# Performance work log

Measured on AMD Instinct MI355X. Metric: run time of the kernel, lower is better.

## Reference

```python
import jax, jax.numpy as jnp
import numpy as np

N_NODES = 50000


def gcn_conv(x, row, col, W, b):
    """PyG GCNConv: add self-loops, symmetric deg^-1/2 normalization,
    linear transform, scatter-add aggregation, bias.
    Self-loop contribution is added analytically (norm = dinv[i]^2)
    instead of appending edges."""
    n = x.shape[0]
    h = x @ W  # [N, out]
    # degree over edges-with-self-loops, counted at target (col)
    deg = jnp.zeros((n,), dtype=x.dtype).at[col].add(1.0) + 1.0
    dinv = jax.lax.rsqrt(deg)  # deg >= 1 thanks to self-loops
    norm = dinv[row] * dinv[col]  # [E]
    # neighbor aggregation: out[col] += norm * h[row]
    agg = jnp.zeros_like(h).at[col].add(norm[:, None] * h[row])
    # self-loop term: dinv[i]^2 * h[i]
    agg = agg + (dinv * dinv)[:, None] * h
    return agg + b


def setup_inputs() -> dict:
    key = jax.random.key(0)
    ks = jax.random.split(key, 8)
    d_in, d_hid, d_out = 128, 128, 128
    n_edges = 625000
    x = jax.random.normal(ks[0], (N_NODES, d_in), dtype=jnp.float32)
    edge_index = jax.random.randint(ks[1], (2, n_edges), 0, N_NODES, dtype=jnp.int64)
    # Glorot-style weights, zero bias (PyG GCNConv defaults)
    def glorot(k, fan_in, fan_out):
        s = jnp.sqrt(6.0 / (fan_in + fan_out)).astype(jnp.float32)
        return jax.random.uniform(k, (fan_in, fan_out), dtype=jnp.float32, minval=-s, maxval=s)
    return {
        "x": x,
        "edge_index": edge_index,
        "W1": glorot(ks[2], d_in, d_hid), "b1": jnp.zeros((d_hid,), jnp.float32),
        "W2": glorot(ks[3], d_hid, d_hid), "b2": jnp.zeros((d_hid,), jnp.float32),
        "W3": glorot(ks[4], d_hid, d_out), "b3": jnp.zeros((d_out,), jnp.float32),
    }


def reference(x, edge_index, W1, b1, W2, b2, W3, b3):
    row, col = edge_index[0], edge_index[1]
    h = jax.nn.relu(gcn_conv(x, row, col, W1, b1))
    h = jax.nn.relu(gcn_conv(h, row, col, W2, b2))
    out = gcn_conv(h, row, col, W3, b3)  # no ReLU on last layer
    return out
```

## Files before the change

### kernel.cpp

```cpp
#include <hip/hip_runtime.h>
#include <hip/hip_fp16.h>

#define NN 50000
#define NE 625000
#define D 128
#define SCAN_BLK 1024
#define NSB ((NN + SCAN_BLK - 1) / SCAN_BLK)

typedef _Float16 half8 __attribute__((ext_vector_type(8)));
typedef float f32x4 __attribute__((ext_vector_type(4)));

union H8U4 { _Float16 h[8]; uint4 u; };


__global__ void zero_kernel(int4* __restrict__ p) {
    int i = blockIdx.x * blockDim.x + threadIdx.x;
    if (i < NN / 4 + 1) p[i] = make_int4(0, 0, 0, 0);
}

__global__ void count_kernel(const int* __restrict__ col, int* __restrict__ counts) {
    int i = blockIdx.x * blockDim.x + threadIdx.x;
    if (i < NE) atomicAdd(&counts[col[i]], 1);
}

__global__ __launch_bounds__(256) void scan1_kernel(const int* __restrict__ counts,
                                                    int* __restrict__ excl,
                                                    int* __restrict__ blocksums) {
    const int b = blockIdx.x, t = threadIdx.x;
    const int base = b * SCAN_BLK + t * 4;
    int v0 = 0, v1 = 0, v2 = 0, v3 = 0;
    if (base + 3 < NN) {
        int4 c = *(const int4*)(counts + base);
        v0 = c.x; v1 = c.y; v2 = c.z; v3 = c.w;
    } else {
        if (base     < NN) v0 = counts[base];
        if (base + 1 < NN) v1 = counts[base + 1];
        if (base + 2 < NN) v2 = counts[base + 2];
        if (base + 3 < NN) v3 = counts[base + 3];
    }
    const int s = v0 + v1 + v2 + v3;
    const int lane = t & 63, wid = t >> 6;
    int inc = s;
    #pragma unroll
    for (int off = 1; off < 64; off <<= 1) {
        int n = __shfl_up(inc, off, 64);
        if (lane >= off) inc += n;
    }
    __shared__ int wsum[4];
    if (lane == 63) wsum[wid] = inc;
    __syncthreads();
    int wbase = 0;
    for (int w = 0; w < wid; w++) wbase += wsum[w];
    const int texcl = wbase + inc - s;
    if (base     < NN) excl[base]     = texcl;
    if (base + 1 < NN) excl[base + 1] = texcl + v0;
    if (base + 2 < NN) excl[base + 2] = texcl + v0 + v1;
    if (base + 3 < NN) excl[base + 3] = texcl + v0 + v1 + v2;
    if (t == 255) blocksums[b] = wbase + inc;
}

__global__ __launch_bounds__(64) void scan2_kernel(const int* __restrict__ blocksums,
                                                   int* __restrict__ blockoff) {
    const int t = threadIdx.x;
    int v = (t < NSB) ? blocksums[t] : 0;
    int inc = v;
    #pragma unroll
    for (int off = 1; off < 64; off <<= 1) {
        int n = __shfl_up(inc, off, 64);
        if (t >= off) inc += n;
    }
    if (t < NSB) blockoff[t] = inc - v;
}

__global__ void scan3_kernel(const int* __restrict__ counts, const int* __restrict__ excl,
                             const int* __restrict__ blockoff, int* __restrict__ offsets,
                             int* __restrict__ cursor, float* __restrict__ dinv) {
    const int i = blockIdx.x * blockDim.x + threadIdx.x;
    if (i < NN) {
        const int o = excl[i] + blockoff[i >> 10];
        offsets[i] = o;
        cursor[i] = o;
        dinv[i] = rsqrtf((float)counts[i] + 1.0f);
    }
    if (i == 0) offsets[NN] = NE;
}

__global__ void fill_kernel(const int* __restrict__ row, const int* __restrict__ col,
                            const float* __restrict__ dinv, int* __restrict__ cursor,
                            uint32_t* __restrict__ csr) {
    int i = blockIdx.x * blockDim.x + threadIdx.x;
    if (i < NE) {
        int r = row[i], c = col[i];
        int p = atomicAdd(&cursor[c], 1);
        __half hw = __float2half_rn(dinv[r] * dinv[c]);
        csr[p] = (uint32_t)r | ((uint32_t)*(const unsigned short*)&hw << 16);
    }
}


__global__ __launch_bounds__(256) void wpack3_kernel(const float* __restrict__ W1,
                                                     const float* __restrict__ W2,
                                                     const float* __restrict__ W3,
                                                     uint4* __restrict__ wp) {
    const int b = blockIdx.x;
    const float* W = (b < 8) ? W1 : (b < 16) ? W2 : W3;
    uint4* dst = wp + (size_t)(b >> 3) * 2048;
    int t = (b & 7) * 256 + threadIdx.x;
    int lane = t & 63, entry = t >> 6;
    int ks = entry >> 3, ctg = entry & 7;
    int j = ctg * 16 + (lane & 15);
    int kb = ks * 32 + (lane >> 4) * 8;
    H8U4 u;
    #pragma unroll
    for (int e = 0; e < 8; e++) u.h[e] = (_Float16)W[(kb + e) * 128 + j];
    dst[t] = u.u;
}


template <bool IN_F16>
__global__ __launch_bounds__(256) void gemm_mfma(const void* __restrict__ Ain,
                                                 const uint4* __restrict__ wpack,
                                                 uint32_t* __restrict__ Hh) {
    __shared__ alignas(16) _Float16 Cs[64][152];
    const int t = threadIdx.x;
    const int w = t >> 6, l = t & 63;
    const int row0 = blockIdx.x * 64;
    const int lr = l & 15;
    const int lg = l >> 4;

    int arow[4];
    #pragma unroll
    for (int rt = 0; rt < 4; rt++) {
        int gr = row0 + rt * 16 + lr;
        arow[rt] = (gr < NN) ? gr : NN - 1;
    }

    f32x4 acc[4][2];
    #pragma unroll
    for (int rt = 0; rt < 4; rt++)
        #pragma unroll
        for (int ct = 0; ct < 2; ct++)
            acc[rt][ct] = (f32x4){0.f, 0.f, 0.f, 0.f};

    #pragma unroll
    for (int ks = 0; ks < 4; ks++) {
        const int kbase = ks * 32 + lg * 8;
        half8 af[4];
        if (IN_F16) {
            const uint4* A = (const uint4*)Ain;
            #pragma unroll
            for (int rt = 0; rt < 4; rt++) {
                H8U4 u;
                u.u = A[arow[rt] * 16 + (kbase >> 3)];
                af[rt] = *(half8*)u.h;
            }
        } else {
            const float4* A = (const float4*)Ain;
            #pragma unroll
            for (int rt = 0; rt < 4; rt++) {
                float4 p0 = A[arow[rt] * 32 + (kbase >> 2)];
                float4 p1 = A[arow[rt] * 32 + (kbase >> 2) + 1];
                half8 h;
                h[0] = (_Float16)p0.x; h[1] = (_Float16)p0.y;
                h[2] = (_Float16)p0.z; h[3] = (_Float16)p0.w;
                h[4] = (_Float16)p1.x; h[5] = (_Float16)p1.y;
                h[6] = (_Float16)p1.z; h[7] = (_Float16)p1.w;
                af[rt] = h;
            }
        }
        half8 bf[2];
        #pragma unroll
        for (int ct = 0; ct < 2; ct++) {
            H8U4 u;
            u.u = wpack[(ks * 8 + (w * 2 + ct)) * 64 + l];
            bf[ct] = *(half8*)u.h;
        }
        #pragma unroll
        for (int rt = 0; rt < 4; rt++)
            #pragma unroll
            for (int ct = 0; ct < 2; ct++)
                acc[rt][ct] = __builtin_amdgcn_mfma_f32_16x16x32_f16(
                    af[rt], bf[ct], acc[rt][ct], 0, 0, 0);
    }

    #pragma unroll
    for (int rt = 0; rt < 4; rt++)
        #pragma unroll
        for (int ct = 0; ct < 2; ct++) {
            const int col = w * 32 + ct * 16 + lr;
            #pragma unroll
            for (int r = 0; r < 4; r++)
                Cs[rt * 16 + lg * 4 + r][col] = (_Float16)acc[rt][ct][r];
        }
    __syncthreads();

    #pragma unroll
    for (int i = t; i < 1024; i += 256) {
        const int row = i >> 4, c16 = i & 15;
        if (row0 + row < NN) {
            uint4 u = *(const uint4*)&Cs[row][c16 * 8];
            *(uint4*)(Hh + (size_t)(row0 + row) * 64 + c16 * 4) = u;
        }
    }
}


static __device__ __forceinline__ void proc4(uint32_t rec, bool valid, int lg,
                                             const uint4* __restrict__ hh4,
                                             float* __restrict__ acc) {
    const int s = (int)(rec & 0xffffu);
    unsigned short wb = (unsigned short)(rec >> 16);
    const float w = valid ? __half2float(*(const __half*)&wb) : 0.0f;
    uint4 v = hh4[(size_t)s * 16 + lg];
    float2 f0 = __half22float2(*(const __half2*)&v.x);
    float2 f1 = __half22float2(*(const __half2*)&v.y);
    float2 f2 = __half22float2(*(const __half2*)&v.z);
    float2 f3 = __half22float2(*(const __half2*)&v.w);
    acc[0] += w * f0.x; acc[1] += w * f0.y;
    acc[2] += w * f1.x; acc[3] += w * f1.y;
    acc[4] += w * f2.x; acc[5] += w * f2.y;
    acc[6] += w * f3.x; acc[7] += w * f3.y;
}

template <bool OUT_F16>
__global__ __launch_bounds__(256) void agg_kernel(const uint4* __restrict__ hh4,
                                                  const int* __restrict__ offsets,
                                                  const uint32_t* __restrict__ csr,
                                                  const float* __restrict__ dinv,
                                                  const float* __restrict__ bias,
                                                  void* __restrict__ out,
                                                  const int relu) {
    const int node = blockIdx.x * 4 + (threadIdx.x >> 6);
    if (node >= NN) return;
    const int l = threadIdx.x & 63;
    const int g = l >> 4;
    const int lg = l & 15;
    const float di = dinv[node];
    const float sw = di * di;
    const int e0 = offsets[node];
    const int e1 = offsets[node + 1];

    float a0[8], a1[8];
    #pragma unroll
    for (int i = 0; i < 8; i++) { a0[i] = 0.f; a1[i] = 0.f; }

    if (e0 < e1) {
        const int elast = e1 - 1;
        uint32_t r0 = csr[min(e0 + g, elast)];
        uint32_t r1 = csr[min(e0 + 4 + g, elast)];
        for (int eb = e0; eb < e1; eb += 8) {
            const int nb = eb + 8;
            uint32_t n0 = csr[min(nb + g, elast)];
            uint32_t n1 = csr[min(nb + 4 + g, elast)];
            proc4(r0, eb + g < e1, lg, hh4, a0);
            proc4(r1, eb + 4 + g < e1, lg, hh4, a1);
            r0 = n0; r1 = n1;
        }
    }

    float s[8];
    #pragma unroll
    for (int i = 0; i < 8; i++) s[i] = a0[i] + a1[i];
    #pragma unroll
    for (int i = 0; i < 8; i++) s[i] += __shfl_xor(s[i], 16, 64);
    #pragma unroll
    for (int i = 0; i < 8; i++) s[i] += __shfl_xor(s[i], 32, 64);

    uint4 sv = hh4[(size_t)node * 16 + lg];
    float2 f0 = __half22float2(*(const __half2*)&sv.x);
    float2 f1 = __half22float2(*(const __half2*)&sv.y);
    float2 f2 = __half22float2(*(const __half2*)&sv.z);
    float2 f3 = __half22float2(*(const __half2*)&sv.w);
    float4 b0 = ((const float4*)bias)[lg * 2];
    float4 b1 = ((const float4*)bias)[lg * 2 + 1];
    s[0] += sw * f0.x + b0.x; s[1] += sw * f0.y + b0.y;
    s[2] += sw * f1.x + b0.z; s[3] += sw * f1.y + b0.w;
    s[4] += sw * f2.x + b1.x; s[5] += sw * f2.y + b1.y;
    s[6] += sw * f3.x + b1.z; s[7] += sw * f3.y + b1.w;
    if (relu) {
        #pragma unroll
        for (int i = 0; i < 8; i++) s[i] = fmaxf(s[i], 0.f);
    }
    if (g == 0) {
        if (OUT_F16) {
            __half2 p0 = __float22half2_rn(make_float2(s[0], s[1]));
            __half2 p1 = __float22half2_rn(make_float2(s[2], s[3]));
            __half2 p2 = __float22half2_rn(make_float2(s[4], s[5]));
            __half2 p3 = __float22half2_rn(make_float2(s[6], s[7]));
            uint4 u;
            u.x = *(const uint32_t*)&p0;
            u.y = *(const uint32_t*)&p1;
            u.z = *(const uint32_t*)&p2;
            u.w = *(const uint32_t*)&p3;
            ((uint4*)out)[(size_t)node * 16 + lg] = u;
        } else {
            float4 o0 = make_float4(s[0], s[1], s[2], s[3]);
            float4 o1 = make_float4(s[4], s[5], s[6], s[7]);
            ((float4*)out)[(size_t)node * 32 + lg * 2] = o0;
            ((float4*)out)[(size_t)node * 32 + lg * 2 + 1] = o1;
        }
    }
}


extern "C" void kernel_launch(void* const* d_in, const int* in_sizes, int n_in,
                              void* d_out, int out_size, void* d_ws, size_t ws_size,
                              hipStream_t stream) {
    (void)in_sizes; (void)n_in; (void)out_size; (void)ws_size;
    const float* x  = (const float*)d_in[0];
    const int*   ei = (const int*)d_in[1];
    const float* W1 = (const float*)d_in[2];
    const float* b1 = (const float*)d_in[3];
    const float* W2 = (const float*)d_in[4];
    const float* b2 = (const float*)d_in[5];
    const float* W3 = (const float*)d_in[6];
    const float* b3 = (const float*)d_in[7];
    const int* row = ei;
    const int* col = ei + NE;
    float* outp = (float*)d_out;

    char* ws = (char*)d_ws;
    size_t off = 0;
    auto walloc = [&](size_t bytes) -> void* {
        void* p = ws + off;
        off = (off + bytes + 255) & ~(size_t)255;
        return p;
    };
    int*      counts   = (int*)walloc(NN * 4 + 16);
    int*      excl     = (int*)walloc(NN * 4);
    int*      blocksums= (int*)walloc(NSB * 4);
    int*      blockoff = (int*)walloc(NSB * 4);
    int*      offsets  = (int*)walloc((NN + 1) * 4);
    int*      cursor   = (int*)walloc(NN * 4);
    float*    dinv     = (float*)walloc(NN * 4);
    uint32_t* csr      = (uint32_t*)walloc((size_t)NE * 4);
    uint32_t* act16    = (uint32_t*)walloc((size_t)NN * D * 2);
    uint32_t* hh16     = (uint32_t*)walloc((size_t)NN * D * 2);
    uint4*    wp       = (uint4*)walloc(3 * 2048 * 16);

    zero_kernel<<<(NN / 4 + 1 + 255) / 256, 256, 0, stream>>>((int4*)counts);
    count_kernel<<<(NE + 255) / 256, 256, 0, stream>>>(col, counts);
    scan1_kernel<<<NSB, 256, 0, stream>>>(counts, excl, blocksums);
    scan2_kernel<<<1, 64, 0, stream>>>(blocksums, blockoff);
    scan3_kernel<<<(NN + 255) / 256, 256, 0, stream>>>(counts, excl, blockoff,
                                                       offsets, cursor, dinv);
    fill_kernel<<<(NE + 255) / 256, 256, 0, stream>>>(row, col, dinv, cursor, csr);
    wpack3_kernel<<<24, 256, 0, stream>>>(W1, W2, W3, wp);

    const int gblocks = (NN + 63) / 64;
    const int ablocks = (NN + 3) / 4;
    const uint4* hh4 = (const uint4*)hh16;
    gemm_mfma<false><<<gblocks, 256, 0, stream>>>(x, wp, hh16);
    agg_kernel<true><<<ablocks, 256, 0, stream>>>(hh4, offsets, csr, dinv, b1, act16, 1);
    gemm_mfma<true><<<gblocks, 256, 0, stream>>>(act16, wp + 2048, hh16);
    agg_kernel<true><<<ablocks, 256, 0, stream>>>(hh4, offsets, csr, dinv, b2, act16, 1);
    gemm_mfma<true><<<gblocks, 256, 0, stream>>>(act16, wp + 4096, hh16);
    agg_kernel<false><<<ablocks, 256, 0, stream>>>(hh4, offsets, csr, dinv, b3, outp, 0);
}
```

Measured before the change: 209.6 us.

## Split feature dimension into column slabs for cache-resident multi-pass aggregation

```diff
diff --git a/kernel.cpp b/kernel.cpp
--- a/kernel.cpp
+++ b/kernel.cpp
@@ -6,11 +6,13 @@
 #define D 128
 #define SCAN_BLK 1024
 #define NSB ((NN + SCAN_BLK - 1) / SCAN_BLK)
+#define NPASS 4
 
 typedef _Float16 half8 __attribute__((ext_vector_type(8)));
 typedef float f32x4 __attribute__((ext_vector_type(4)));
-
-union H8U4 { _Float16 h[8]; uint4 u; };
+typedef unsigned int u32x4 __attribute__((ext_vector_type(4)));
+
+union H8U4 { _Float16 h[8]; uint4 u; u32x4 v; };
 
 
 __global__ void zero_kernel(int4* __restrict__ p) {
@@ -120,7 +122,7 @@
 template <bool IN_F16>
 __global__ __launch_bounds__(256) void gemm_mfma(const void* __restrict__ Ain,
                                                  const uint4* __restrict__ wpack,
-                                                 uint32_t* __restrict__ Hh) {
+                                                 unsigned int* __restrict__ Hs) {
     __shared__ alignas(16) _Float16 Cs[64][152];
     const int t = threadIdx.x;
     const int w = t >> 6, l = t & 63;
@@ -144,17 +146,17 @@
 
     #pragma unroll
     for (int ks = 0; ks < 4; ks++) {
-        const int kbase = ks * 32 + lg * 8;
         half8 af[4];
         if (IN_F16) {
             const uint4* A = (const uint4*)Ain;
             #pragma unroll
             for (int rt = 0; rt < 4; rt++) {
                 H8U4 u;
-                u.u = A[arow[rt] * 16 + (kbase >> 3)];
+                u.u = A[(size_t)ks * NN * 4 + arow[rt] * 4 + lg];
                 af[rt] = *(half8*)u.h;
             }
         } else {
+            const int kbase = ks * 32 + lg * 8;
             const float4* A = (const float4*)Ain;
             #pragma unroll
             for (int rt = 0; rt < 4; rt++) {
@@ -198,20 +200,22 @@
     for (int i = t; i < 1024; i += 256) {
         const int row = i >> 4, c16 = i & 15;
         if (row0 + row < NN) {
-            uint4 u = *(const uint4*)&Cs[row][c16 * 8];
-            *(uint4*)(Hh + (size_t)(row0 + row) * 64 + c16 * 4) = u;
-        }
-    }
-}
-
-
-static __device__ __forceinline__ void proc4(uint32_t rec, bool valid, int lg,
-                                             const uint4* __restrict__ hh4,
-                                             float* __restrict__ acc) {
+            u32x4 u = *(const u32x4*)&Cs[row][c16 * 8];
+            u32x4* dst = (u32x4*)Hs + (size_t)(c16 >> 2) * NN * 4 +
+                         (size_t)(row0 + row) * 4 + (c16 & 3);
+            __builtin_nontemporal_store(u, dst);
+        }
+    }
+}
+
+
+static __device__ __forceinline__ void proc16(uint32_t rec, bool valid, int q,
+                                              const uint4* __restrict__ hsp,
+                                              float* __restrict__ acc) {
     const int s = (int)(rec & 0xffffu);
     unsigned short wb = (unsigned short)(rec >> 16);
     const float w = valid ? __half2float(*(const __half*)&wb) : 0.0f;
-    uint4 v = hh4[(size_t)s * 16 + lg];
+    uint4 v = hsp[(size_t)s * 4 + q];
     float2 f0 = __half22float2(*(const __half2*)&v.x);
     float2 f1 = __half22float2(*(const __half2*)&v.y);
     float2 f2 = __half22float2(*(const __half2*)&v.z);
@@ -223,18 +227,19 @@
 }
 
 template <bool OUT_F16>
-__global__ __launch_bounds__(256) void agg_kernel(const uint4* __restrict__ hh4,
-                                                  const int* __restrict__ offsets,
-                                                  const uint32_t* __restrict__ csr,
-                                                  const float* __restrict__ dinv,
-                                                  const float* __restrict__ bias,
-                                                  void* __restrict__ out,
-                                                  const int relu) {
+__global__ __launch_bounds__(256) void agg_pass(const uint4* __restrict__ hs,
+                                                const int* __restrict__ offsets,
+                                                const uint32_t* __restrict__ csr,
+                                                const float* __restrict__ dinv,
+                                                const float* __restrict__ bias,
+                                                void* __restrict__ out,
+                                                const int relu, const int pass) {
     const int node = blockIdx.x * 4 + (threadIdx.x >> 6);
     if (node >= NN) return;
     const int l = threadIdx.x & 63;
-    const int g = l >> 4;
-    const int lg = l & 15;
+    const int g = l >> 2;
+    const int q = l & 3;
+    const uint4* hsp = hs + (size_t)pass * NN * 4;
     const float di = dinv[node];
     const float sw = di * di;
     const int e0 = offsets[node];
@@ -246,14 +251,14 @@
 
     if (e0 < e1) {
         const int elast = e1 - 1;
-        uint32_t r0 = csr[min(e0 + g, elast)];
-        uint32_t r1 = csr[min(e0 + 4 + g, elast)];
-        for (int eb = e0; eb < e1; eb += 8) {
-            const int nb = eb + 8;
-            uint32_t n0 = csr[min(nb + g, elast)];
-            uint32_t n1 = csr[min(nb + 4 + g, elast)];
-            proc4(r0, eb + g < e1, lg, hh4, a0);
-            proc4(r1, eb + 4 + g < e1, lg, hh4, a1);
+        uint32_t r0 = __builtin_nontemporal_load(csr + min(e0 + g, elast));
+        uint32_t r1 = __builtin_nontemporal_load(csr + min(e0 + 16 + g, elast));
+        for (int eb = e0; eb < e1; eb += 32) {
+            const int nb = eb + 32;
+            uint32_t n0 = __builtin_nontemporal_load(csr + min(nb + g, elast));
+            uint32_t n1 = __builtin_nontemporal_load(csr + min(nb + 16 + g, elast));
+            proc16(r0, eb + g < e1, q, hsp, a0);
+            proc16(r1, eb + 16 + g < e1, q, hsp, a1);
             r0 = n0; r1 = n1;
         }
     }
@@ -262,17 +267,20 @@
     #pragma unroll
     for (int i = 0; i < 8; i++) s[i] = a0[i] + a1[i];
     #pragma unroll
-    for (int i = 0; i < 8; i++) s[i] += __shfl_xor(s[i], 16, 64);
-    #pragma unroll
-    for (int i = 0; i < 8; i++) s[i] += __shfl_xor(s[i], 32, 64);
-
-    uint4 sv = hh4[(size_t)node * 16 + lg];
+    for (int i = 0; i < 8; i++) {
+        s[i] += __shfl_xor(s[i], 4, 64);
+        s[i] += __shfl_xor(s[i], 8, 64);
+        s[i] += __shfl_xor(s[i], 16, 64);
+        s[i] += __shfl_xor(s[i], 32, 64);
+    }
+
+    uint4 sv = hsp[(size_t)node * 4 + q];
     float2 f0 = __half22float2(*(const __half2*)&sv.x);
     float2 f1 = __half22float2(*(const __half2*)&sv.y);
     float2 f2 = __half22float2(*(const __half2*)&sv.z);
     float2 f3 = __half22float2(*(const __half2*)&sv.w);
-    float4 b0 = ((const float4*)bias)[lg * 2];
-    float4 b1 = ((const float4*)bias)[lg * 2 + 1];
+    float4 b0 = ((const float4*)bias)[pass * 8 + q * 2];
+    float4 b1 = ((const float4*)bias)[pass * 8 + q * 2 + 1];
     s[0] += sw * f0.x + b0.x; s[1] += sw * f0.y + b0.y;
     s[2] += sw * f1.x + b0.z; s[3] += sw * f1.y + b0.w;
     s[4] += sw * f2.x + b1.x; s[5] += sw * f2.y + b1.y;
@@ -287,17 +295,19 @@
             __half2 p1 = __float22half2_rn(make_float2(s[2], s[3]));
             __half2 p2 = __float22half2_rn(make_float2(s[4], s[5]));
             __half2 p3 = __float22half2_rn(make_float2(s[6], s[7]));
-            uint4 u;
+            u32x4 u;
             u.x = *(const uint32_t*)&p0;
             u.y = *(const uint32_t*)&p1;
             u.z = *(const uint32_t*)&p2;
             u.w = *(const uint32_t*)&p3;
-            ((uint4*)out)[(size_t)node * 16 + lg] = u;
+            u32x4* dst = (u32x4*)out + (size_t)pass * NN * 4 + (size_t)node * 4 + q;
+            __builtin_nontemporal_store(u, dst);
         } else {
-            float4 o0 = make_float4(s[0], s[1], s[2], s[3]);
-            float4 o1 = make_float4(s[4], s[5], s[6], s[7]);
-            ((float4*)out)[(size_t)node * 32 + lg * 2] = o0;
-            ((float4*)out)[(size_t)node * 32 + lg * 2 + 1] = o1;
+            f32x4 o0 = {s[0], s[1], s[2], s[3]};
+            f32x4 o1 = {s[4], s[5], s[6], s[7]};
+            f32x4* dst = (f32x4*)out + (size_t)node * 32 + pass * 8 + q * 2;
+            __builtin_nontemporal_store(o0, dst);
+            __builtin_nontemporal_store(o1, dst + 1);
         }
     }
 }
@@ -334,8 +344,8 @@
     int*      cursor   = (int*)walloc(NN * 4);
     float*    dinv     = (float*)walloc(NN * 4);
     uint32_t* csr      = (uint32_t*)walloc((size_t)NE * 4);
-    uint32_t* act16    = (uint32_t*)walloc((size_t)NN * D * 2);
-    uint32_t* hh16     = (uint32_t*)walloc((size_t)NN * D * 2);
+    uint4*    act16    = (uint4*)walloc((size_t)NN * D * 2);
+    uint4*    hh16     = (uint4*)walloc((size_t)NN * D * 2);
     uint4*    wp       = (uint4*)walloc(3 * 2048 * 16);
 
     zero_kernel<<<(NN / 4 + 1 + 255) / 256, 256, 0, stream>>>((int4*)counts);
@@ -349,11 +359,13 @@
 
     const int gblocks = (NN + 63) / 64;
     const int ablocks = (NN + 3) / 4;
-    const uint4* hh4 = (const uint4*)hh16;
-    gemm_mfma<false><<<gblocks, 256, 0, stream>>>(x, wp, hh16);
-    agg_kernel<true><<<ablocks, 256, 0, stream>>>(hh4, offsets, csr, dinv, b1, act16, 1);
-    gemm_mfma<true><<<gblocks, 256, 0, stream>>>(act16, wp + 2048, hh16);
-    agg_kernel<true><<<ablocks, 256, 0, stream>>>(hh4, offsets, csr, dinv, b2, act16, 1);
-    gemm_mfma<true><<<gblocks, 256, 0, stream>>>(act16, wp + 4096, hh16);
-    agg_kernel<false><<<ablocks, 256, 0, stream>>>(hh4, offsets, csr, dinv, b3, outp, 0);
-}
+    gemm_mfma<false><<<gblocks, 256, 0, stream>>>(x, wp, (unsigned int*)hh16);
+    for (int p = 0; p < NPASS; p++)
+        agg_pass<true><<<ablocks, 256, 0, stream>>>(hh16, offsets, csr, dinv, b1, act16, 1, p);
+    gemm_mfma<true><<<gblocks, 256, 0, stream>>>(act16, wp + 2048, (unsigned int*)hh16);
+    for (int p = 0; p < NPASS; p++)
+        agg_pass<true><<<ablocks, 256, 0, stream>>>(hh16, offsets, csr, dinv, b2, act16, 1, p);
+    gemm_mfma<true><<<gblocks, 256, 0, stream>>>(act16, wp + 4096, (unsigned int*)hh16);
+    for (int p = 0; p < NPASS; p++)
+        agg_pass<false><<<ablocks, 256, 0, stream>>>(hh16, offsets, csr, dinv, b3, outp, 0, p);
+}
```

New measurement: 356.8 us. 70.2% more time.
